# Optimization experiments

Measured on AMD Instinct MI355X. Metric: run time of the kernel, lower is better.

The kernel has to match this reference:

```python
import jax, jax.numpy as jnp
import numpy as np

C = 256
G = 32  # groups
EPS = 1e-5

def _xavier(key, shape, gain=1.0):
    fan_in, fan_out = shape[1], shape[0]
    a = gain * np.sqrt(6.0 / (fan_in + fan_out))
    return jax.random.uniform(key, shape, jnp.float32, -a, a)

def setup_inputs() -> dict:
    key = jax.random.key(0)
    ks = jax.random.split(key, 5)
    x = jax.random.normal(ks[0], (2, C, 16, 16, 16), jnp.float32)
    return {
        "x": x,
        "gn_gamma": jnp.ones((C,), jnp.float32),
        "gn_beta": jnp.zeros((C,), jnp.float32),
        "Wq": _xavier(ks[1], (C, C)), "bq": jnp.zeros((C,), jnp.float32),
        "Wk": _xavier(ks[2], (C, C)), "bk": jnp.zeros((C,), jnp.float32),
        "Wv": _xavier(ks[3], (C, C)), "bv": jnp.zeros((C,), jnp.float32),
        "Wp": _xavier(ks[4], (C, C), gain=1e-05), "bp": jnp.zeros((C,), jnp.float32),
    }

def reference(x, gn_gamma, gn_beta, Wq, bq, Wk, bk, Wv, bv, Wp, bp):
    B, Cc, D, H, W = x.shape
    N = D * H * W
    xf = x.reshape(B, Cc, N)  # [B, C, N]
    # GroupNorm over (C//G, N) per group
    xg = xf.reshape(B, G, Cc // G, N)
    mu = jnp.mean(xg, axis=(2, 3), keepdims=True)
    var = jnp.var(xg, axis=(2, 3), keepdims=True)
    h = ((xg - mu) * jax.lax.rsqrt(var + EPS)).reshape(B, Cc, N)
    h = h * gn_gamma[None, :, None] + gn_beta[None, :, None]
    # 1x1x1 convs == channel matmuls
    q = jnp.einsum('oc,bcn->bno', Wq, h) + bq  # [B, N, C]
    k = jnp.einsum('oc,bcn->bon', Wk, h) + bk[None, :, None]  # [B, C, N]
    v = jnp.einsum('oc,bcn->bno', Wv, h) + bv  # [B, N, C]
    scale = float(Cc) ** (-0.5)
    w = jnp.einsum('bnc,bcm->bnm', q, k) * scale  # [B, N, N]
    w = jax.nn.softmax(w, axis=-1)
    a = jnp.einsum('bnm,bmc->bnc', w, v)  # [B, N, C]
    out = jnp.einsum('oc,bnc->bon', Wp, a) + bp[None, :, None]  # [B, C, N]
    return x + out.reshape(B, Cc, D, H, W)
```

## Files before the change

### kernel.cpp

```cpp
#include <hip/hip_runtime.h>
#include <stdint.h>

#define B_ 2
#define C_ 256
#define N_ 4096
#define EPS_ 1e-5f

typedef short short8 __attribute__((ext_vector_type(8)));
typedef float f32x4 __attribute__((ext_vector_type(4)));
typedef float f32x16 __attribute__((ext_vector_type(16)));
typedef long long i64;

static __device__ __forceinline__ unsigned short f2bf(float f) {
    union { float f; unsigned int u; } v; v.f = f;
    unsigned int r = v.u + 0x7FFF + ((v.u >> 16) & 1);
    return (unsigned short)(r >> 16);
}
static __device__ __forceinline__ float bf2f(unsigned short u) {
    union { unsigned int u; float f; } v; v.u = ((unsigned int)u) << 16;
    return v.f;
}
static __device__ __forceinline__ unsigned char f2fp8(float f) {
    return (unsigned char)(__builtin_amdgcn_cvt_pk_fp8_f32(f, f, 0, false) & 0xff);
}
static __device__ __forceinline__ unsigned char f2bf8(float f) {
    return (unsigned char)(__builtin_amdgcn_cvt_pk_bf8_f32(f, f, 0, false) & 0xff);
}

__global__ void gn_stats(const float* __restrict__ x, float2* __restrict__ stats) {
    const float4* p = reinterpret_cast<const float4*>(x + (size_t)blockIdx.x * 32768);
    float s = 0.f, ss = 0.f;
    for (int i = threadIdx.x; i < 8192; i += 256) {
        float4 v = p[i];
        s  += v.x + v.y + v.z + v.w;
        ss += v.x*v.x + v.y*v.y + v.z*v.z + v.w*v.w;
    }
    for (int m = 32; m; m >>= 1) { s += __shfl_down(s, m, 64); ss += __shfl_down(ss, m, 64); }
    __shared__ float as_[4], as2_[4];
    int w = threadIdx.x >> 6;
    if ((threadIdx.x & 63) == 0) { as_[w] = s; as2_[w] = ss; }
    __syncthreads();
    if (threadIdx.x == 0) {
        float S = as_[0]+as_[1]+as_[2]+as_[3], SS = as2_[0]+as2_[1]+as2_[2]+as2_[3];
        float mu = S / 32768.f;
        float var = SS / 32768.f - mu*mu;
        stats[blockIdx.x] = make_float2(mu, rsqrtf(var + EPS_));
    }
}

__global__ void wconv(const float* __restrict__ a, const float* __restrict__ b,
                      const float* __restrict__ c, const float* __restrict__ d,
                      ushort* __restrict__ o) {
    int t = blockIdx.x * 256 + threadIdx.x;
    int idx = t * 4;
    const float* src = (idx >> 16) == 0 ? a : (idx >> 16) == 1 ? b : (idx >> 16) == 2 ? c : d;
    float4 v = *reinterpret_cast<const float4*>(src + (idx & 65535));
    ushort4 r; r.x = f2bf(v.x); r.y = f2bf(v.y); r.z = f2bf(v.z); r.w = f2bf(v.w);
    *reinterpret_cast<ushort4*>(o + idx) = r;
}

__global__ void gnorm_t(const float* __restrict__ x, const float2* __restrict__ stats,
                        const float* __restrict__ gamma, const float* __restrict__ beta,
                        ushort* __restrict__ ht) {
    __shared__ float tile[32][33];
    int b = blockIdx.z, n0 = blockIdx.x * 32, c0 = blockIdx.y * 32;
    int tx = threadIdx.x, ty = threadIdx.y;
    #pragma unroll
    for (int i = 0; i < 4; i++) {
        int c = c0 + ty + i*8;
        float2 st = stats[b*32 + (c >> 3)];
        float v = x[((size_t)(b*C_ + c))*N_ + n0 + tx];
        tile[ty + i*8][tx] = (v - st.x) * st.y * gamma[c] + beta[c];
    }
    __syncthreads();
    #pragma unroll
    for (int i = 0; i < 4; i++) {
        int n = n0 + ty + i*8;
        ht[((size_t)(b*N_ + n))*C_ + c0 + tx] = f2bf(tile[tx][ty + i*8]);
    }
}

template<bool BIAS_ROW, int OMODE>
__global__ __launch_bounds__(256) void gemm_nt(
    const ushort* __restrict__ A, const ushort* __restrict__ Bm,
    const float* __restrict__ bias, const float* __restrict__ resid,
    void* __restrict__ outp,
    long aBatch, long bBatch, long oBatch, long rBatch, int ldo)
{
    __shared__ ushort sA[64][72];
    __shared__ ushort sB[64][72];
    int bz = blockIdx.z;
    const ushort* Ab = A + (size_t)aBatch * bz;
    const ushort* Bb = Bm + (size_t)bBatch * bz;
    int i0 = blockIdx.x * 64, j0 = blockIdx.y * 64;
    int tid = threadIdx.x, w = tid >> 6, lane = tid & 63, lr = lane & 15, lg = lane >> 4;
    f32x4 acc[4] = {};
    for (int ks = 0; ks < 256; ks += 64) {
        #pragma unroll
        for (int it = 0; it < 2; it++) {
            int ch = tid + it*256;
            int row = ch >> 3, cc = ch & 7;
            *reinterpret_cast<uint4*>(&sA[row][cc*8]) =
                *reinterpret_cast<const uint4*>(Ab + ((size_t)(i0 + row))*256 + ks + cc*8);
            *reinterpret_cast<uint4*>(&sB[row][cc*8]) =
                *reinterpret_cast<const uint4*>(Bb + ((size_t)(j0 + row))*256 + ks + cc*8);
        }
        __syncthreads();
        #pragma unroll
        for (int kc = 0; kc < 2; kc++) {
            short8 af = *reinterpret_cast<const short8*>(&sA[w*16 + lr][kc*32 + lg*8]);
            #pragma unroll
            for (int cb = 0; cb < 4; cb++) {
                short8 bf = *reinterpret_cast<const short8*>(&sB[cb*16 + lr][kc*32 + lg*8]);
                acc[cb] = __builtin_amdgcn_mfma_f32_16x16x32_bf16(af, bf, acc[cb], 0, 0, 0);
            }
        }
        __syncthreads();
    }
    #pragma unroll
    for (int cb = 0; cb < 4; cb++) {
        #pragma unroll
        for (int r = 0; r < 4; r++) {
            int i = i0 + w*16 + lg*4 + r;
            int j = j0 + cb*16 + lr;
            float v = acc[cb][r] + (BIAS_ROW ? bias[i] : bias[j]);
            size_t oidx = (size_t)oBatch*bz + (size_t)i*ldo + j;
            if (OMODE == 2) {
                ((float*)outp)[oidx] = v + resid[(size_t)rBatch*bz + (size_t)i*ldo + j];
            } else if (OMODE == 1) {
                ((unsigned char*)outp)[oidx] = f2fp8(v);
            } else {
                ((ushort*)outp)[oidx] = f2bf(v);
            }
        }
    }
}

__global__ __launch_bounds__(256) void qkproj(
    const ushort* __restrict__ ht, const ushort* __restrict__ wq, const ushort* __restrict__ wk,
    const float* __restrict__ bq, const float* __restrict__ bk,
    unsigned char* __restrict__ qo, unsigned char* __restrict__ ko)
{
    __shared__ ushort sA[64][72], sBq[64][72], sBk[64][72];
    int bz = blockIdx.z;
    const ushort* Ab = ht + (size_t)bz * N_ * C_;
    int i0 = blockIdx.x * 64, j0 = blockIdx.y * 64;
    int tid = threadIdx.x, w = tid >> 6, lane = tid & 63, lr = lane & 15, lg = lane >> 4;
    f32x4 aq[4] = {}, ak[4] = {};
    for (int ks = 0; ks < 256; ks += 64) {
        #pragma unroll
        for (int it = 0; it < 2; it++) {
            int ch = tid + it*256;
            int row = ch >> 3, cc = ch & 7;
            *reinterpret_cast<uint4*>(&sA[row][cc*8]) =
                *reinterpret_cast<const uint4*>(Ab + ((size_t)(i0 + row))*256 + ks + cc*8);
            *reinterpret_cast<uint4*>(&sBq[row][cc*8]) =
                *reinterpret_cast<const uint4*>(wq + ((size_t)(j0 + row))*256 + ks + cc*8);
            *reinterpret_cast<uint4*>(&sBk[row][cc*8]) =
                *reinterpret_cast<const uint4*>(wk + ((size_t)(j0 + row))*256 + ks + cc*8);
        }
        __syncthreads();
        #pragma unroll
        for (int kc = 0; kc < 2; kc++) {
            short8 af = *reinterpret_cast<const short8*>(&sA[w*16 + lr][kc*32 + lg*8]);
            #pragma unroll
            for (int cb = 0; cb < 4; cb++) {
                short8 b1 = *reinterpret_cast<const short8*>(&sBq[cb*16 + lr][kc*32 + lg*8]);
                short8 b2 = *reinterpret_cast<const short8*>(&sBk[cb*16 + lr][kc*32 + lg*8]);
                aq[cb] = __builtin_amdgcn_mfma_f32_16x16x32_bf16(af, b1, aq[cb], 0, 0, 0);
                ak[cb] = __builtin_amdgcn_mfma_f32_16x16x32_bf16(af, b2, ak[cb], 0, 0, 0);
            }
        }
        __syncthreads();
    }
    #pragma unroll
    for (int cb = 0; cb < 4; cb++) {
        #pragma unroll
        for (int r = 0; r < 4; r++) {
            int i = i0 + w*16 + lg*4 + r;
            int j = j0 + cb*16 + lr;
            size_t oidx = ((size_t)(bz*N_ + i))*256 + j;
            qo[oidx] = f2fp8(aq[cb][r] + bq[j]);
            ko[oidx] = f2fp8(ak[cb][r] + bk[j]);
        }
    }
}

#define FLASH_LDS 79872
__global__ __launch_bounds__(256, 2) void flash4(
    const unsigned char* __restrict__ q, const unsigned char* __restrict__ k,
    const unsigned char* __restrict__ vT,
    ushort* __restrict__ Opart, float* __restrict__ lsum, ushort* __restrict__ aout, int nsplit)
{
    extern __shared__ char smem[];
    int b = blockIdx.z, s = blockIdx.y, qt = blockIdx.x;
    int tid = threadIdx.x, w = tid >> 6, lane = tid & 63;
    int l31 = lane & 31, hi = lane >> 5;
    int nrow0 = qt*128 + w*32;
    const unsigned char* kB = k  + (size_t)b * N_ * 256;
    const unsigned char* vB = vT + (size_t)b * 256 * N_;

    i64 qf[16];
    #pragma unroll
    for (int kc = 0; kc < 16; kc++)
        qf[kc] = *reinterpret_cast<const i64*>(
            q + ((size_t)(b*N_) + nrow0 + l31)*256 + kc*16 + hi*8);

    f32x16 oacc[8] = {};
    float lpart[16] = {};

    int tiles = 64 / nsplit;
    int t0 = s * tiles;

    char* kbuf0 = smem;
    char* vbuf0 = smem + 33792;
    char* pw    = smem + 70656 + w*2304;

    uint4 kreg[4], vreg[4];
    auto loadKV = [&](int t) {
        #pragma unroll
        for (int i = 0; i < 4; i++) {
            int row = w*16 + i*4 + (lane >> 4);
            kreg[i] = *reinterpret_cast<const uint4*>(
                kB + (size_t)(t*64 + row)*256 + (lane & 15)*16);
        }
        #pragma unroll
        for (int i = 0; i < 4; i++) {
            int c = w*64 + i*16 + (lane >> 2);
            vreg[i] = *reinterpret_cast<const uint4*>(
                vB + (size_t)c*4096 + t*64 + (lane & 3)*16);
        }
    };
    auto writeKV = [&](int sel) {
        #pragma unroll
        for (int i = 0; i < 4; i++) {
            int row = w*16 + i*4 + (lane >> 4);
            char* p = kbuf0 + sel*16896 + row*264 + (lane & 15)*16;
            *reinterpret_cast<uint2*>(p)     = make_uint2(kreg[i].x, kreg[i].y);
            *reinterpret_cast<uint2*>(p + 8) = make_uint2(kreg[i].z, kreg[i].w);
        }
        #pragma unroll
        for (int i = 0; i < 4; i++) {
            int c = w*64 + i*16 + (lane >> 2);
            char* p = vbuf0 + sel*18432 + c*72 + (lane & 3)*16;
            *reinterpret_cast<uint2*>(p)     = make_uint2(vreg[i].x, vreg[i].y);
            *reinterpret_cast<uint2*>(p + 8) = make_uint2(vreg[i].z, vreg[i].w);
        }
    };

    loadKV(t0);
    writeKV(0);
    __syncthreads();
    int sel = 0;

    for (int ti = 0; ti < tiles; ti++) {
        int t = t0 + ti;
        int tn = (ti + 1 < tiles) ? t + 1 : t0;
        loadKV(tn);

        const char* kb_ = kbuf0 + sel*16896;
        f32x16 s0 = {}, s1 = {};
        #pragma unroll
        for (int kc = 0; kc < 16; kc++) {
            i64 b0 = *reinterpret_cast<const i64*>(kb_ + l31*264        + kc*16 + hi*8);
            i64 b1 = *reinterpret_cast<const i64*>(kb_ + (l31+32)*264   + kc*16 + hi*8);
            s0 = __builtin_amdgcn_mfma_f32_32x32x16_fp8_fp8(qf[kc], b0, s0, 0, 0, 0);
            s1 = __builtin_amdgcn_mfma_f32_32x32x16_fp8_fp8(qf[kc], b1, s1, 0, 0, 0);
        }

        #pragma unroll
        for (int r = 0; r < 16; r++) {
            int R = (r & 3) + 8*(r >> 2) + 4*hi;
            float p0 = __expf(fminf(s0[r]*0.0625f, 10.5f));
            float p1 = __expf(fminf(s1[r]*0.0625f, 10.5f));
            lpart[r] += p0 + p1;
            *(unsigned char*)(pw + R*72 + l31)      = f2bf8(p0);
            *(unsigned char*)(pw + R*72 + 32 + l31) = f2bf8(p1);
        }

        const char* vb_ = vbuf0 + sel*18432;
        i64 pa[4];
        #pragma unroll
        for (int ks = 0; ks < 4; ks++)
            pa[ks] = *reinterpret_cast<const i64*>(pw + l31*72 + ks*16 + hi*8);
        #pragma unroll
        for (int cb = 0; cb < 8; cb++) {
            #pragma unroll
            for (int ks = 0; ks < 4; ks++) {
                i64 bv = *reinterpret_cast<const i64*>(vb_ + (cb*32 + l31)*72 + ks*16 + hi*8);
                oacc[cb] = __builtin_amdgcn_mfma_f32_32x32x16_bf8_fp8(pa[ks], bv, oacc[cb], 0, 0, 0);
            }
        }

        writeKV(sel ^ 1);
        __syncthreads();
        sel ^= 1;
    }

    #pragma unroll
    for (int r = 0; r < 16; r++) {
        float v = lpart[r];
        v += __shfl_xor(v, 1, 64);
        v += __shfl_xor(v, 2, 64);
        v += __shfl_xor(v, 4, 64);
        v += __shfl_xor(v, 8, 64);
        v += __shfl_xor(v, 16, 64);
        lpart[r] = v;
    }

    if (nsplit == 1) {
        #pragma unroll
        for (int r = 0; r < 16; r++) {
            int R = (r & 3) + 8*(r >> 2) + 4*hi;
            float inv = 1.f / lpart[r];
            #pragma unroll
            for (int cb = 0; cb < 8; cb++)
                aout[((size_t)(b*N_) + nrow0 + R)*256 + cb*32 + l31] = f2bf(oacc[cb][r] * inv);
        }
    } else {
        size_t obase = ((size_t)(b*nsplit + s)*N_ + nrow0) * 256;
        #pragma unroll
        for (int r = 0; r < 16; r++) {
            int R = (r & 3) + 8*(r >> 2) + 4*hi;
            #pragma unroll
            for (int cb = 0; cb < 8; cb++)
                Opart[obase + (size_t)R*256 + cb*32 + l31] = f2bf(oacc[cb][r]);
        }
        if (l31 == 0) {
            #pragma unroll
            for (int r = 0; r < 16; r++)
                lsum[(size_t)(b*nsplit + s)*N_ + nrow0 + (r & 3) + 8*(r >> 2) + 4*hi] = lpart[r];
        }
    }
}

__global__ void combine2(const ushort* __restrict__ Opart, const float* __restrict__ lsum,
                         ushort* __restrict__ aout, int nsplit) {
    int g = threadIdx.x >> 6, lane = threadIdx.x & 63;
    int idx = blockIdx.x*4 + g;
    int b = idx >> 12, n = idx & 4095;
    float L = 0.f;
    for (int s2 = 0; s2 < nsplit; s2++) L += lsum[(size_t)(b*nsplit + s2)*N_ + n];
    float inv = 1.f / L;
    float a0 = 0.f, a1 = 0.f, a2 = 0.f, a3 = 0.f;
    for (int s2 = 0; s2 < nsplit; s2++) {
        ushort4 o = *reinterpret_cast<const ushort4*>(
            Opart + ((size_t)(b*nsplit + s2)*N_ + n)*256 + lane*4);
        a0 += bf2f(o.x); a1 += bf2f(o.y); a2 += bf2f(o.z); a3 += bf2f(o.w);
    }
    ushort4 r; r.x = f2bf(a0*inv); r.y = f2bf(a1*inv); r.z = f2bf(a2*inv); r.w = f2bf(a3*inv);
    *reinterpret_cast<ushort4*>(aout + (size_t)idx*256 + lane*4) = r;
}

extern "C" void kernel_launch(void* const* d_in, const int* in_sizes, int n_in,
                              void* d_out, int out_size, void* d_ws, size_t ws_size,
                              hipStream_t stream) {
    const float* x     = (const float*)d_in[0];
    const float* gamma = (const float*)d_in[1];
    const float* beta  = (const float*)d_in[2];
    const float* Wq = (const float*)d_in[3]; const float* bq = (const float*)d_in[4];
    const float* Wk = (const float*)d_in[5]; const float* bk = (const float*)d_in[6];
    const float* Wv = (const float*)d_in[7]; const float* bv = (const float*)d_in[8];
    const float* Wp = (const float*)d_in[9]; const float* bp = (const float*)d_in[10];
    float* out = (float*)d_out;

    char* ws = (char*)d_ws;
    float2* stats = (float2*)ws;
    ushort* wqb = (ushort*)(ws + 1024);
    ushort* wkb = wqb + 65536;
    ushort* wvb = wkb + 65536;
    ushort* wpb = wvb + 65536;
    ushort* ht  = (ushort*)(ws + 1024 + 524288);
    const size_t NB = (size_t)B_ * N_ * C_;
    unsigned char* qb  = (unsigned char*)(ht + NB);
    unsigned char* kb8 = qb  + NB;
    unsigned char* vTb = kb8 + NB;
    ushort* ab = (ushort*)(vTb + NB);
    char* after = (char*)(ab + NB);
    float*  lsum  = (float*)after;
    ushort* Opart = (ushort*)(after + 262144);

    int nsplit = (ws_size >= (size_t)48*1024*1024) ? 8 : 4;

    hipFuncSetAttribute((const void*)flash4, hipFuncAttributeMaxDynamicSharedMemorySize,
                        FLASH_LDS);

    gn_stats<<<64, 256, 0, stream>>>(x, stats);
    wconv<<<256, 256, 0, stream>>>(Wq, Wk, Wv, Wp, wqb);
    gnorm_t<<<dim3(128, 8, 2), dim3(32, 8), 0, stream>>>(x, stats, gamma, beta, ht);
    qkproj<<<dim3(64, 4, 2), 256, 0, stream>>>(ht, wqb, wkb, bq, bk, qb, kb8);
    gemm_nt<true, 1><<<dim3(4, 64, 2), 256, 0, stream>>>(wvb, ht, bv, nullptr, vTb,
        0, (long)N_*C_, (long)C_*N_, 0, N_);
    flash4<<<dim3(32, nsplit, 2), 256, FLASH_LDS, stream>>>(qb, kb8, vTb, Opart, lsum, ab, nsplit);
    combine2<<<2048, 256, 0, stream>>>(Opart, lsum, ab, nsplit);
    gemm_nt<true, 2><<<dim3(4, 64, 2), 256, 0, stream>>>(wpb, ab, bp, x, out,
        0, (long)N_*C_, (long)C_*N_, (long)C_*N_, N_);
}
```

Before: 90.21 us.

## Fuse prep kernels and V projection into QK projection, add MFMA priority hints

Merges the GroupNorm statistics and weight conversion into one launch, and folds the V projection into the Q/K projection kernel. V is now written transposed in fp8 with a permuted column order inside each 64-wide block, presumably matching the order the flash kernel reads. The flash kernel raises wave priority around its MFMA loops and packs two bf8 probability values per store. This removes two launches and one re-read of the normalized activations, at the cost of scattered byte stores for V and more LDS per projection block.

```diff
diff --git a/kernel.cpp b/kernel.cpp
--- a/kernel.cpp
+++ b/kernel.cpp
@@ -23,40 +23,44 @@
 static __device__ __forceinline__ unsigned char f2fp8(float f) {
     return (unsigned char)(__builtin_amdgcn_cvt_pk_fp8_f32(f, f, 0, false) & 0xff);
 }
-static __device__ __forceinline__ unsigned char f2bf8(float f) {
-    return (unsigned char)(__builtin_amdgcn_cvt_pk_bf8_f32(f, f, 0, false) & 0xff);
-}
-
-__global__ void gn_stats(const float* __restrict__ x, float2* __restrict__ stats) {
-    const float4* p = reinterpret_cast<const float4*>(x + (size_t)blockIdx.x * 32768);
-    float s = 0.f, ss = 0.f;
-    for (int i = threadIdx.x; i < 8192; i += 256) {
-        float4 v = p[i];
-        s  += v.x + v.y + v.z + v.w;
-        ss += v.x*v.x + v.y*v.y + v.z*v.z + v.w*v.w;
-    }
-    for (int m = 32; m; m >>= 1) { s += __shfl_down(s, m, 64); ss += __shfl_down(ss, m, 64); }
+static __device__ __forceinline__ unsigned short pk_bf8(float a, float b) {
+    return (unsigned short)(__builtin_amdgcn_cvt_pk_bf8_f32(a, b, 0, false) & 0xffff);
+}
+
+__global__ __launch_bounds__(256) void prep(
+    const float* __restrict__ x, float2* __restrict__ stats,
+    const float* __restrict__ Wq, const float* __restrict__ Wk,
+    const float* __restrict__ Wv, const float* __restrict__ Wp,
+    ushort* __restrict__ o)
+{
     __shared__ float as_[4], as2_[4];
-    int w = threadIdx.x >> 6;
-    if ((threadIdx.x & 63) == 0) { as_[w] = s; as2_[w] = ss; }
-    __syncthreads();
-    if (threadIdx.x == 0) {
-        float S = as_[0]+as_[1]+as_[2]+as_[3], SS = as2_[0]+as2_[1]+as2_[2]+as2_[3];
-        float mu = S / 32768.f;
-        float var = SS / 32768.f - mu*mu;
-        stats[blockIdx.x] = make_float2(mu, rsqrtf(var + EPS_));
-    }
-}
-
-__global__ void wconv(const float* __restrict__ a, const float* __restrict__ b,
-                      const float* __restrict__ c, const float* __restrict__ d,
-                      ushort* __restrict__ o) {
-    int t = blockIdx.x * 256 + threadIdx.x;
-    int idx = t * 4;
-    const float* src = (idx >> 16) == 0 ? a : (idx >> 16) == 1 ? b : (idx >> 16) == 2 ? c : d;
-    float4 v = *reinterpret_cast<const float4*>(src + (idx & 65535));
-    ushort4 r; r.x = f2bf(v.x); r.y = f2bf(v.y); r.z = f2bf(v.z); r.w = f2bf(v.w);
-    *reinterpret_cast<ushort4*>(o + idx) = r;
+    if (blockIdx.x < 64) {
+        const float4* p = reinterpret_cast<const float4*>(x + (size_t)blockIdx.x * 32768);
+        float s = 0.f, ss = 0.f;
+        for (int i = threadIdx.x; i < 8192; i += 256) {
+            float4 v = p[i];
+            s  += v.x + v.y + v.z + v.w;
+            ss += v.x*v.x + v.y*v.y + v.z*v.z + v.w*v.w;
+        }
+        for (int m = 32; m; m >>= 1) { s += __shfl_down(s, m, 64); ss += __shfl_down(ss, m, 64); }
+        int w = threadIdx.x >> 6;
+        if ((threadIdx.x & 63) == 0) { as_[w] = s; as2_[w] = ss; }
+        __syncthreads();
+        if (threadIdx.x == 0) {
+            float S = as_[0]+as_[1]+as_[2]+as_[3], SS = as2_[0]+as2_[1]+as2_[2]+as2_[3];
+            float mu = S / 32768.f;
+            float var = SS / 32768.f - mu*mu;
+            stats[blockIdx.x] = make_float2(mu, rsqrtf(var + EPS_));
+        }
+    } else {
+        int t = (blockIdx.x - 64) * 256 + threadIdx.x;
+        int idx = t * 4;
+        int sel = idx >> 16;
+        const float* src = sel == 0 ? Wq : sel == 1 ? Wk : sel == 2 ? Wv : Wp;
+        float4 v = *reinterpret_cast<const float4*>(src + (idx & 65535));
+        ushort4 r; r.x = f2bf(v.x); r.y = f2bf(v.y); r.z = f2bf(v.z); r.w = f2bf(v.w);
+        *reinterpret_cast<ushort4*>(o + idx) = r;
+    }
 }
 
 __global__ void gnorm_t(const float* __restrict__ x, const float2* __restrict__ stats,
@@ -80,73 +84,18 @@
     }
 }
 
-template<bool BIAS_ROW, int OMODE>
-__global__ __launch_bounds__(256) void gemm_nt(
-    const ushort* __restrict__ A, const ushort* __restrict__ Bm,
-    const float* __restrict__ bias, const float* __restrict__ resid,
-    void* __restrict__ outp,
-    long aBatch, long bBatch, long oBatch, long rBatch, int ldo)
+__global__ __launch_bounds__(256) void qkvproj(
+    const ushort* __restrict__ ht, const ushort* __restrict__ wq,
+    const ushort* __restrict__ wk, const ushort* __restrict__ wv,
+    const float* __restrict__ bq, const float* __restrict__ bk, const float* __restrict__ bv,
+    unsigned char* __restrict__ qo, unsigned char* __restrict__ ko, unsigned char* __restrict__ vo)
 {
-    __shared__ ushort sA[64][72];
-    __shared__ ushort sB[64][72];
-    int bz = blockIdx.z;
-    const ushort* Ab = A + (size_t)aBatch * bz;
-    const ushort* Bb = Bm + (size_t)bBatch * bz;
-    int i0 = blockIdx.x * 64, j0 = blockIdx.y * 64;
-    int tid = threadIdx.x, w = tid >> 6, lane = tid & 63, lr = lane & 15, lg = lane >> 4;
-    f32x4 acc[4] = {};
-    for (int ks = 0; ks < 256; ks += 64) {
-        #pragma unroll
-        for (int it = 0; it < 2; it++) {
-            int ch = tid + it*256;
-            int row = ch >> 3, cc = ch & 7;
-            *reinterpret_cast<uint4*>(&sA[row][cc*8]) =
-                *reinterpret_cast<const uint4*>(Ab + ((size_t)(i0 + row))*256 + ks + cc*8);
-            *reinterpret_cast<uint4*>(&sB[row][cc*8]) =
-                *reinterpret_cast<const uint4*>(Bb + ((size_t)(j0 + row))*256 + ks + cc*8);
-        }
-        __syncthreads();
-        #pragma unroll
-        for (int kc = 0; kc < 2; kc++) {
-            short8 af = *reinterpret_cast<const short8*>(&sA[w*16 + lr][kc*32 + lg*8]);
-            #pragma unroll
-            for (int cb = 0; cb < 4; cb++) {
-                short8 bf = *reinterpret_cast<const short8*>(&sB[cb*16 + lr][kc*32 + lg*8]);
-                acc[cb] = __builtin_amdgcn_mfma_f32_16x16x32_bf16(af, bf, acc[cb], 0, 0, 0);
-            }
-        }
-        __syncthreads();
-    }
-    #pragma unroll
-    for (int cb = 0; cb < 4; cb++) {
-        #pragma unroll
-        for (int r = 0; r < 4; r++) {
-            int i = i0 + w*16 + lg*4 + r;
-            int j = j0 + cb*16 + lr;
-            float v = acc[cb][r] + (BIAS_ROW ? bias[i] : bias[j]);
-            size_t oidx = (size_t)oBatch*bz + (size_t)i*ldo + j;
-            if (OMODE == 2) {
-                ((float*)outp)[oidx] = v + resid[(size_t)rBatch*bz + (size_t)i*ldo + j];
-            } else if (OMODE == 1) {
-                ((unsigned char*)outp)[oidx] = f2fp8(v);
-            } else {
-                ((ushort*)outp)[oidx] = f2bf(v);
-            }
-        }
-    }
-}
-
-__global__ __launch_bounds__(256) void qkproj(
-    const ushort* __restrict__ ht, const ushort* __restrict__ wq, const ushort* __restrict__ wk,
-    const float* __restrict__ bq, const float* __restrict__ bk,
-    unsigned char* __restrict__ qo, unsigned char* __restrict__ ko)
-{
-    __shared__ ushort sA[64][72], sBq[64][72], sBk[64][72];
+    __shared__ ushort sA[64][72], sBq[64][72], sBk[64][72], sBv[64][72];
     int bz = blockIdx.z;
     const ushort* Ab = ht + (size_t)bz * N_ * C_;
     int i0 = blockIdx.x * 64, j0 = blockIdx.y * 64;
     int tid = threadIdx.x, w = tid >> 6, lane = tid & 63, lr = lane & 15, lg = lane >> 4;
-    f32x4 aq[4] = {}, ak[4] = {};
+    f32x4 aq[4] = {}, ak[4] = {}, av[4] = {};
     for (int ks = 0; ks < 256; ks += 64) {
         #pragma unroll
         for (int it = 0; it < 2; it++) {
@@ -158,6 +107,8 @@
                 *reinterpret_cast<const uint4*>(wq + ((size_t)(j0 + row))*256 + ks + cc*8);
             *reinterpret_cast<uint4*>(&sBk[row][cc*8]) =
                 *reinterpret_cast<const uint4*>(wk + ((size_t)(j0 + row))*256 + ks + cc*8);
+            *reinterpret_cast<uint4*>(&sBv[row][cc*8]) =
+                *reinterpret_cast<const uint4*>(wv + ((size_t)(j0 + row))*256 + ks + cc*8);
         }
         __syncthreads();
         #pragma unroll
@@ -167,8 +118,10 @@
             for (int cb = 0; cb < 4; cb++) {
                 short8 b1 = *reinterpret_cast<const short8*>(&sBq[cb*16 + lr][kc*32 + lg*8]);
                 short8 b2 = *reinterpret_cast<const short8*>(&sBk[cb*16 + lr][kc*32 + lg*8]);
+                short8 b3 = *reinterpret_cast<const short8*>(&sBv[cb*16 + lr][kc*32 + lg*8]);
                 aq[cb] = __builtin_amdgcn_mfma_f32_16x16x32_bf16(af, b1, aq[cb], 0, 0, 0);
                 ak[cb] = __builtin_amdgcn_mfma_f32_16x16x32_bf16(af, b2, ak[cb], 0, 0, 0);
+                av[cb] = __builtin_amdgcn_mfma_f32_16x16x32_bf16(af, b3, av[cb], 0, 0, 0);
             }
         }
         __syncthreads();
@@ -182,12 +135,15 @@
             size_t oidx = ((size_t)(bz*N_ + i))*256 + j;
             qo[oidx] = f2fp8(aq[cb][r] + bq[j]);
             ko[oidx] = f2fp8(ak[cb][r] + bk[j]);
+            int m = i & 63;
+            int col = (i & ~63) + ((m & 31)*2 + (m >> 5));
+            vo[((size_t)bz*C_ + j)*N_ + col] = f2fp8(av[cb][r] + bv[j]);
         }
     }
 }
 
 #define FLASH_LDS 79872
-__global__ __launch_bounds__(256, 2) void flash4(
+__global__ __launch_bounds__(256, 2) void flash5(
     const unsigned char* __restrict__ q, const unsigned char* __restrict__ k,
     const unsigned char* __restrict__ vT,
     ushort* __restrict__ Opart, float* __restrict__ lsum, ushort* __restrict__ aout, int nsplit)
@@ -260,6 +216,7 @@
 
         const char* kb_ = kbuf0 + sel*16896;
         f32x16 s0 = {}, s1 = {};
+        __builtin_amdgcn_s_setprio(1);
         #pragma unroll
         for (int kc = 0; kc < 16; kc++) {
             i64 b0 = *reinterpret_cast<const i64*>(kb_ + l31*264        + kc*16 + hi*8);
@@ -267,6 +224,7 @@
             s0 = __builtin_amdgcn_mfma_f32_32x32x16_fp8_fp8(qf[kc], b0, s0, 0, 0, 0);
             s1 = __builtin_amdgcn_mfma_f32_32x32x16_fp8_fp8(qf[kc], b1, s1, 0, 0, 0);
         }
+        __builtin_amdgcn_s_setprio(0);
 
         #pragma unroll
         for (int r = 0; r < 16; r++) {
@@ -274,8 +232,7 @@
             float p0 = __expf(fminf(s0[r]*0.0625f, 10.5f));
             float p1 = __expf(fminf(s1[r]*0.0625f, 10.5f));
             lpart[r] += p0 + p1;
-            *(unsigned char*)(pw + R*72 + l31)      = f2bf8(p0);
-            *(unsigned char*)(pw + R*72 + 32 + l31) = f2bf8(p1);
+            *(ushort*)(pw + R*72 + l31*2) = pk_bf8(p0, p1);
         }
 
         const char* vb_ = vbuf0 + sel*18432;
@@ -283,6 +240,7 @@
         #pragma unroll
         for (int ks = 0; ks < 4; ks++)
             pa[ks] = *reinterpret_cast<const i64*>(pw + l31*72 + ks*16 + hi*8);
+        __builtin_amdgcn_s_setprio(1);
         #pragma unroll
         for (int cb = 0; cb < 8; cb++) {
             #pragma unroll
@@ -291,6 +249,7 @@
                 oacc[cb] = __builtin_amdgcn_mfma_f32_32x32x16_bf8_fp8(pa[ks], bv, oacc[cb], 0, 0, 0);
             }
         }
+        __builtin_amdgcn_s_setprio(0);
 
         writeKV(sel ^ 1);
         __syncthreads();
@@ -350,6 +309,52 @@
     }
     ushort4 r; r.x = f2bf(a0*inv); r.y = f2bf(a1*inv); r.z = f2bf(a2*inv); r.w = f2bf(a3*inv);
     *reinterpret_cast<ushort4*>(aout + (size_t)idx*256 + lane*4) = r;
+}
+
+__global__ __launch_bounds__(256) void pgemm(
+    const ushort* __restrict__ A, const ushort* __restrict__ Bm,
+    const float* __restrict__ bias, const float* __restrict__ resid,
+    float* __restrict__ outp, long bBatch, long oBatch)
+{
+    __shared__ ushort sA[64][72];
+    __shared__ ushort sB[64][72];
+    int bz = blockIdx.z;
+    const ushort* Bb = Bm + (size_t)bBatch * bz;
+    int i0 = blockIdx.x * 64, j0 = blockIdx.y * 64;
+    int tid = threadIdx.x, w = tid >> 6, lane = tid & 63, lr = lane & 15, lg = lane >> 4;
+    f32x4 acc[4] = {};
+    for (int ks = 0; ks < 256; ks += 64) {
+        #pragma unroll
+        for (int it = 0; it < 2; it++) {
+            int ch = tid + it*256;
+            int row = ch >> 3, cc = ch & 7;
+            *reinterpret_cast<uint4*>(&sA[row][cc*8]) =
+                *reinterpret_cast<const uint4*>(A + ((size_t)(i0 + row))*256 + ks + cc*8);
+            *reinterpret_cast<uint4*>(&sB[row][cc*8]) =
+                *reinterpret_cast<const uint4*>(Bb + ((size_t)(j0 + row))*256 + ks + cc*8);
+        }
+        __syncthreads();
+        #pragma unroll
+        for (int kc = 0; kc < 2; kc++) {
+            short8 af = *reinterpret_cast<const short8*>(&sA[w*16 + lr][kc*32 + lg*8]);
+            #pragma unroll
+            for (int cb = 0; cb < 4; cb++) {
+                short8 bf = *reinterpret_cast<const short8*>(&sB[cb*16 + lr][kc*32 + lg*8]);
+                acc[cb] = __builtin_amdgcn_mfma_f32_16x16x32_bf16(af, bf, acc[cb], 0, 0, 0);
+            }
+        }
+        __syncthreads();
+    }
+    #pragma unroll
+    for (int cb = 0; cb < 4; cb++) {
+        #pragma unroll
+        for (int r = 0; r < 4; r++) {
+            int i = i0 + w*16 + lg*4 + r;
+            int j = j0 + cb*16 + lr;
+            size_t oidx = (size_t)oBatch*bz + (size_t)i*N_ + j;
+            outp[oidx] = acc[cb][r] + bias[i] + resid[oidx];
+        }
+    }
 }
 
 extern "C" void kernel_launch(void* const* d_in, const int* in_sizes, int n_in,
@@ -382,17 +387,13 @@
 
     int nsplit = (ws_size >= (size_t)48*1024*1024) ? 8 : 4;
 
-    hipFuncSetAttribute((const void*)flash4, hipFuncAttributeMaxDynamicSharedMemorySize,
+    hipFuncSetAttribute((const void*)flash5, hipFuncAttributeMaxDynamicSharedMemorySize,
                         FLASH_LDS);
 
-    gn_stats<<<64, 256, 0, stream>>>(x, stats);
-    wconv<<<256, 256, 0, stream>>>(Wq, Wk, Wv, Wp, wqb);
+    prep<<<320, 256, 0, stream>>>(x, stats, Wq, Wk, Wv, Wp, wqb);
     gnorm_t<<<dim3(128, 8, 2), dim3(32, 8), 0, stream>>>(x, stats, gamma, beta, ht);
-    qkproj<<<dim3(64, 4, 2), 256, 0, stream>>>(ht, wqb, wkb, bq, bk, qb, kb8);
-    gemm_nt<true, 1><<<dim3(4, 64, 2), 256, 0, stream>>>(wvb, ht, bv, nullptr, vTb,
-        0, (long)N_*C_, (long)C_*N_, 0, N_);
-    flash4<<<dim3(32, nsplit, 2), 256, FLASH_LDS, stream>>>(qb, kb8, vTb, Opart, lsum, ab, nsplit);
+    qkvproj<<<dim3(64, 4, 2), 256, 0, stream>>>(ht, wqb, wkb, wvb, bq, bk, bv, qb, kb8, vTb);
+    flash5<<<dim3(32, nsplit, 2), 256, FLASH_LDS, stream>>>(qb, kb8, vTb, Opart, lsum, ab, nsplit);
     combine2<<<2048, 256, 0, stream>>>(Opart, lsum, ab, nsplit);
-    gemm_nt<true, 2><<<dim3(4, 64, 2), 256, 0, stream>>>(wpb, ab, bp, x, out,
-        0, (long)N_*C_, (long)C_*N_, (long)C_*N_, N_);
-}
+    pgemm<<<dim3(4, 64, 2), 256, 0, stream>>>(wpb, ab, bp, x, out, (long)N_*C_, (long)C_*N_);
+}
```

Result: faster. 84.47 us (-6.4%).
